# Kernel tuning notes

Measured on AMD Instinct MI355X. Metric: run time of the kernel, lower is better.

Reference implementation:

```python
import jax, jax.numpy as jnp
import numpy as np

WINDOW_SIZE = 5  # hardcoded in module __init__


def local_window_mask(T, dtype=jnp.float32):
    # Faithful to torch code: start from triu(ones, diagonal=1) (value 1.0 for
    # j > i, NOT -inf!), then set entries outside the band |j - i| <= sz to -inf.
    sz = WINDOW_SIZE // 2
    i = jnp.arange(T)[:, None]
    j = jnp.arange(T)[None, :]
    upper = (j > i).astype(dtype)            # triu part contributes +1 bias
    in_band = jnp.abs(j - i) <= sz
    return jnp.where(in_band, upper, jnp.float32(-jnp.inf).astype(dtype))


def setup_inputs() -> dict:
    key = jax.random.key(0)
    kx, kq, kk, kv = jax.random.split(key, 4)
    B, T, C = 4, 4096, 64
    head_size = 64
    s = 1.0 / np.sqrt(C)
    return {
        "x": jax.random.normal(kx, (B, T, C), dtype=jnp.float32),
        "Wq": jax.random.normal(kq, (head_size, C), dtype=jnp.float32) * s,
        "Wk": jax.random.normal(kk, (head_size, C), dtype=jnp.float32) * s,
        "Wv": jax.random.normal(kv, (head_size, C), dtype=jnp.float32) * s,
    }


def reference(x, Wq, Wk, Wv):
    B, T, C = x.shape
    # nn.Linear(d_model, head_size, bias=False): y = x @ W.T
    q = jnp.einsum('btc,hc->bth', x, Wq)
    k = jnp.einsum('btc,hc->bth', x, Wk)
    v = jnp.einsum('btc,hc->bth', x, Wv)
    scale = jnp.asarray(C, x.dtype) ** -0.5   # scale uses input dim C
    scores = jnp.einsum('bth,bsh->bts', q, k) * scale + local_window_mask(T, x.dtype)
    attn = jax.nn.softmax(scores, axis=-1)    # original computes this twice; once suffices (same math)
    op = jnp.einsum('bts,bsh->bth', attn, v)
    return (op, attn)
```

## Files before the change

### kernel.cpp

```cpp
#include <hip/hip_runtime.h>

constexpr int B      = 4;
constexpr int T      = 4096;
constexpr int C      = 64;
constexpr int H      = 64;
constexpr int TILE   = 32;
constexpr int HALO   = 2;
constexpr int HR     = TILE + 2 * HALO;
constexpr int LS     = 68;
constexpr int NT     = 256;
constexpr int NTILES = T / TILE;
constexpr int CBLOCKS = B * NTILES;
constexpr int FBLOCKS = 2048;
constexpr int GRID    = CBLOCKS + FBLOCKS;
constexpr int T4     = T / 4;
constexpr unsigned TOTAL4 = (unsigned)B * (unsigned)T * (unsigned)T4;

__global__ __launch_bounds__(NT, 4)
void sparse_attn_fused(const float* __restrict__ x,
                       const float* __restrict__ Wq,
                       const float* __restrict__ Wk,
                       const float* __restrict__ Wv,
                       float* __restrict__ out)
{
    __shared__ float sX[HR][LS];
    __shared__ float sW[C][LS];
    __shared__ float sU[TILE][LS];
    __shared__ float sS[TILE][8];

    const int tid = threadIdx.x;
    const unsigned bid = blockIdx.x;
    const size_t attnBase = (size_t)B * T * H;

    if (bid % 5u != 0u) {
        const unsigned fid = bid - bid / 5u - 1u;
        float4* __restrict__ attn4 = (float4*)(out + attnBase);
        const unsigned base   = fid * NT + tid;
        const unsigned stride = (unsigned)FBLOCKS * NT;
        const float4 z = make_float4(0.f, 0.f, 0.f, 0.f);
        for (unsigned n = base; n < TOTAL4; n += stride) {
            const int c4 = (int)(n & (T4 - 1));
            const int i  = (int)((n >> 10) & (T - 1));
            const int j0 = c4 << 2;
            if (j0 > i + HALO || j0 + 3 < i - HALO) attn4[n] = z;
        }
        return;
    }

    const unsigned cid = bid / 5u;
    const int b    = (int)(cid / NTILES);
    const int tile = (int)(cid % NTILES);
    const int row0 = tile * TILE;
    const float* xb = x + (size_t)b * T * C;

    for (int s = tid; s < HR * (C / 4); s += NT) {
        const int lr = s >> 4;
        const int c4 = (s & 15) << 2;
        const int gr = row0 + lr - HALO;
        float4 v = make_float4(0.f, 0.f, 0.f, 0.f);
        if (gr >= 0 && gr < T) v = *(const float4*)(xb + (size_t)gr * C + c4);
        *(float4*)&sX[lr][c4] = v;
    }
    {
        const int c   = tid >> 2;
        const int cp0 = (tid & 3) << 4;
        float acc[16];
#pragma unroll
        for (int j = 0; j < 16; ++j) acc[j] = 0.f;
#pragma unroll 4
        for (int h = 0; h < C; ++h) {
            const float  wq = Wq[h * 64 + c];
            const float4 k0 = *(const float4*)&Wk[h * 64 + cp0];
            const float4 k1 = *(const float4*)&Wk[h * 64 + cp0 + 4];
            const float4 k2 = *(const float4*)&Wk[h * 64 + cp0 + 8];
            const float4 k3 = *(const float4*)&Wk[h * 64 + cp0 + 12];
            acc[0]  = fmaf(wq, k0.x, acc[0]);  acc[1]  = fmaf(wq, k0.y, acc[1]);
            acc[2]  = fmaf(wq, k0.z, acc[2]);  acc[3]  = fmaf(wq, k0.w, acc[3]);
            acc[4]  = fmaf(wq, k1.x, acc[4]);  acc[5]  = fmaf(wq, k1.y, acc[5]);
            acc[6]  = fmaf(wq, k1.z, acc[6]);  acc[7]  = fmaf(wq, k1.w, acc[7]);
            acc[8]  = fmaf(wq, k2.x, acc[8]);  acc[9]  = fmaf(wq, k2.y, acc[9]);
            acc[10] = fmaf(wq, k2.z, acc[10]); acc[11] = fmaf(wq, k2.w, acc[11]);
            acc[12] = fmaf(wq, k3.x, acc[12]); acc[13] = fmaf(wq, k3.y, acc[13]);
            acc[14] = fmaf(wq, k3.z, acc[14]); acc[15] = fmaf(wq, k3.w, acc[15]);
        }
#pragma unroll
        for (int j = 0; j < 4; ++j)
            *(float4*)&sW[c][cp0 + 4 * j] =
                make_float4(acc[4*j], acc[4*j+1], acc[4*j+2], acc[4*j+3]);
    }
    __syncthreads();

    {
        const int r0 = tid >> 4;
        const int h0 = (tid & 15) << 2;
        float acc[2][4];
#pragma unroll
        for (int k = 0; k < 2; ++k)
#pragma unroll
            for (int j = 0; j < 4; ++j) acc[k][j] = 0.f;
        for (int c4 = 0; c4 < C; c4 += 4) {
            const float4 xa = *(const float4*)&sX[r0 + HALO][c4];
            const float4 xc = *(const float4*)&sX[r0 + 16 + HALO][c4];
#pragma unroll
            for (int cc = 0; cc < 4; ++cc) {
                const float4 wv = *(const float4*)&sW[c4 + cc][h0];
                const float xs0 = (&xa.x)[cc];
                const float xs1 = (&xc.x)[cc];
                acc[0][0] = fmaf(xs0, wv.x, acc[0][0]);
                acc[0][1] = fmaf(xs0, wv.y, acc[0][1]);
                acc[0][2] = fmaf(xs0, wv.z, acc[0][2]);
                acc[0][3] = fmaf(xs0, wv.w, acc[0][3]);
                acc[1][0] = fmaf(xs1, wv.x, acc[1][0]);
                acc[1][1] = fmaf(xs1, wv.y, acc[1][1]);
                acc[1][2] = fmaf(xs1, wv.z, acc[1][2]);
                acc[1][3] = fmaf(xs1, wv.w, acc[1][3]);
            }
        }
        *(float4*)&sU[r0][h0]      = make_float4(acc[0][0], acc[0][1], acc[0][2], acc[0][3]);
        *(float4*)&sU[r0 + 16][h0] = make_float4(acc[1][0], acc[1][1], acc[1][2], acc[1][3]);
    }
    __syncthreads();

    if (tid < TILE) {
        const int i  = tid;
        const int ig = row0 + i;
        float sc[5];
        float m = -__builtin_inff();
#pragma unroll
        for (int d = 0; d < 5; ++d) {
            const int jg = ig - HALO + d;
            float v = -__builtin_inff();
            if (jg >= 0 && jg < T) {
                float a = 0.f;
#pragma unroll
                for (int c4 = 0; c4 < C; c4 += 4) {
                    const float4 u  = *(const float4*)&sU[i][c4];
                    const float4 xk = *(const float4*)&sX[i + d][c4];
                    a += u.x * xk.x + u.y * xk.y + u.z * xk.z + u.w * xk.w;
                }
                v = a * 0.125f + (d > 2 ? 1.0f : 0.0f);
            }
            sc[d] = v;
            m = fmaxf(m, v);
        }
        float p[5];
        float sum = 0.f;
#pragma unroll
        for (int d = 0; d < 5; ++d) { p[d] = expf(sc[d] - m); sum += p[d]; }
        const float inv = 1.f / sum;
#pragma unroll
        for (int d = 0; d < 5; ++d) sS[i][d] = p[d] * inv;

        float* rowp = out + attnBase + ((size_t)b * T + ig) * T;
        const int cLo = (ig - HALO > 0 ? ig - HALO : 0) >> 2;
        const int cHi = (ig + HALO < T - 1 ? ig + HALO : T - 1) >> 2;
        for (int cch = cLo; cch <= cHi; ++cch) {
            float vv[4];
#pragma unroll
            for (int q = 0; q < 4; ++q) {
                const int d = (cch << 2) + q - (ig - HALO);
                vv[q] = (d >= 0 && d < 5) ? sS[i][d] : 0.f;
            }
            *(float4*)(rowp + (cch << 2)) = make_float4(vv[0], vv[1], vv[2], vv[3]);
        }
    }
    if (tid >= 64) {
        for (int s = tid - 64; s < C * H; s += NT - 64)
            sW[s & 63][s >> 6] = Wv[s];
    }
    __syncthreads();

    {
        const int i  = tid >> 3;
        const int c0 = (tid & 7) << 3;
        float y[8];
#pragma unroll
        for (int j = 0; j < 8; ++j) y[j] = 0.f;
#pragma unroll
        for (int d = 0; d < 5; ++d) {
            const float pd = sS[i][d];
            const float4 a = *(const float4*)&sX[i + d][c0];
            const float4 b2 = *(const float4*)&sX[i + d][c0 + 4];
            y[0] = fmaf(pd, a.x, y[0]);  y[1] = fmaf(pd, a.y, y[1]);
            y[2] = fmaf(pd, a.z, y[2]);  y[3] = fmaf(pd, a.w, y[3]);
            y[4] = fmaf(pd, b2.x, y[4]); y[5] = fmaf(pd, b2.y, y[5]);
            y[6] = fmaf(pd, b2.z, y[6]); y[7] = fmaf(pd, b2.w, y[7]);
        }
        *(float4*)&sU[i][c0]     = make_float4(y[0], y[1], y[2], y[3]);
        *(float4*)&sU[i][c0 + 4] = make_float4(y[4], y[5], y[6], y[7]);
    }
    __syncthreads();

    {
        const int r0 = tid >> 4;
        const int h0 = (tid & 15) << 2;
        float acc[2][4];
#pragma unroll
        for (int k = 0; k < 2; ++k)
#pragma unroll
            for (int j = 0; j < 4; ++j) acc[k][j] = 0.f;
        for (int c4 = 0; c4 < C; c4 += 4) {
            const float4 ya = *(const float4*)&sU[r0][c4];
            const float4 yc = *(const float4*)&sU[r0 + 16][c4];
#pragma unroll
            for (int cc = 0; cc < 4; ++cc) {
                const float4 wv = *(const float4*)&sW[c4 + cc][h0];
                const float ys0 = (&ya.x)[cc];
                const float ys1 = (&yc.x)[cc];
                acc[0][0] = fmaf(ys0, wv.x, acc[0][0]);
                acc[0][1] = fmaf(ys0, wv.y, acc[0][1]);
                acc[0][2] = fmaf(ys0, wv.z, acc[0][2]);
                acc[0][3] = fmaf(ys0, wv.w, acc[0][3]);
                acc[1][0] = fmaf(ys1, wv.x, acc[1][0]);
                acc[1][1] = fmaf(ys1, wv.y, acc[1][1]);
                acc[1][2] = fmaf(ys1, wv.z, acc[1][2]);
                acc[1][3] = fmaf(ys1, wv.w, acc[1][3]);
            }
        }
        float* o = out + ((size_t)b * T + row0) * H;
        *(float4*)&o[(size_t)r0 * H + h0] =
            make_float4(acc[0][0], acc[0][1], acc[0][2], acc[0][3]);
        *(float4*)&o[(size_t)(r0 + 16) * H + h0] =
            make_float4(acc[1][0], acc[1][1], acc[1][2], acc[1][3]);
    }
}

extern "C" void kernel_launch(void* const* d_in, const int* in_sizes, int n_in,
                              void* d_out, int out_size, void* d_ws, size_t ws_size,
                              hipStream_t stream) {
    (void)in_sizes; (void)n_in; (void)d_ws; (void)ws_size; (void)out_size;
    const float* x  = (const float*)d_in[0];
    const float* Wq = (const float*)d_in[1];
    const float* Wk = (const float*)d_in[2];
    const float* Wv = (const float*)d_in[3];
    float* out = (float*)d_out;
    sparse_attn_fused<<<dim3(GRID), dim3(NT), 0, stream>>>(x, Wq, Wk, Wv, out);
}
```

Before: 324.1 us.

## Replace in-kernel attention zero-fill with hipMemsetAsync plus compute-only kernel

Drops the fused fill blocks that wrote zeros outside the band of the attention matrix. Instead the whole attention buffer is zeroed with hipMemsetAsync, and a separate kernel then runs only the band-compute blocks. The memset writes the full matrix, band included, so the band is written twice. The fill and the compute can no longer overlap, in exchange for a write path that may be better tuned.

```diff
diff --git a/kernel.cpp b/kernel.cpp
--- a/kernel.cpp
+++ b/kernel.cpp
@@ -11,17 +11,13 @@
 constexpr int NT     = 256;
 constexpr int NTILES = T / TILE;
 constexpr int CBLOCKS = B * NTILES;
-constexpr int FBLOCKS = 2048;
-constexpr int GRID    = CBLOCKS + FBLOCKS;
-constexpr int T4     = T / 4;
-constexpr unsigned TOTAL4 = (unsigned)B * (unsigned)T * (unsigned)T4;
 
 __global__ __launch_bounds__(NT, 4)
-void sparse_attn_fused(const float* __restrict__ x,
-                       const float* __restrict__ Wq,
-                       const float* __restrict__ Wk,
-                       const float* __restrict__ Wv,
-                       float* __restrict__ out)
+void sparse_attn_compute(const float* __restrict__ x,
+                         const float* __restrict__ Wq,
+                         const float* __restrict__ Wk,
+                         const float* __restrict__ Wv,
+                         float* __restrict__ out)
 {
     __shared__ float sX[HR][LS];
     __shared__ float sW[C][LS];
@@ -29,27 +25,10 @@
     __shared__ float sS[TILE][8];
 
     const int tid = threadIdx.x;
-    const unsigned bid = blockIdx.x;
     const size_t attnBase = (size_t)B * T * H;
 
-    if (bid % 5u != 0u) {
-        const unsigned fid = bid - bid / 5u - 1u;
-        float4* __restrict__ attn4 = (float4*)(out + attnBase);
-        const unsigned base   = fid * NT + tid;
-        const unsigned stride = (unsigned)FBLOCKS * NT;
-        const float4 z = make_float4(0.f, 0.f, 0.f, 0.f);
-        for (unsigned n = base; n < TOTAL4; n += stride) {
-            const int c4 = (int)(n & (T4 - 1));
-            const int i  = (int)((n >> 10) & (T - 1));
-            const int j0 = c4 << 2;
-            if (j0 > i + HALO || j0 + 3 < i - HALO) attn4[n] = z;
-        }
-        return;
-    }
-
-    const unsigned cid = bid / 5u;
-    const int b    = (int)(cid / NTILES);
-    const int tile = (int)(cid % NTILES);
+    const int b    = (int)(blockIdx.x / NTILES);
+    const int tile = (int)(blockIdx.x % NTILES);
     const int row0 = tile * TILE;
     const float* xb = x + (size_t)b * T * C;
 
@@ -179,7 +158,7 @@
 #pragma unroll
         for (int d = 0; d < 5; ++d) {
             const float pd = sS[i][d];
-            const float4 a = *(const float4*)&sX[i + d][c0];
+            const float4 a  = *(const float4*)&sX[i + d][c0];
             const float4 b2 = *(const float4*)&sX[i + d][c0 + 4];
             y[0] = fmaf(pd, a.x, y[0]);  y[1] = fmaf(pd, a.y, y[1]);
             y[2] = fmaf(pd, a.z, y[2]);  y[3] = fmaf(pd, a.w, y[3]);
@@ -234,5 +213,9 @@
     const float* Wk = (const float*)d_in[2];
     const float* Wv = (const float*)d_in[3];
     float* out = (float*)d_out;
-    sparse_attn_fused<<<dim3(GRID), dim3(NT), 0, stream>>>(x, Wq, Wk, Wv, out);
+
+    float* attn = out + (size_t)B * T * H;
+    (void)hipMemsetAsync((void*)attn, 0, (size_t)B * T * T * sizeof(float), stream);
+
+    sparse_attn_compute<<<dim3(CBLOCKS), dim3(NT), 0, stream>>>(x, Wq, Wk, Wv, out);
 }
```

Result: faster. 311.1 us (-4.0%).
